# Performance work log

Hardware: AMD Instinct MI355X
Metric: run time of the kernel (lower is better)

## Reference

```python
import jax, jax.numpy as jnp
import numpy as np

H = 16
D_MODEL = 1024
D_K = D_MODEL // H


def setup_inputs() -> dict:
    key = jax.random.key(0)
    ks = jax.random.split(key, 11)
    B, S = 2, 2048
    scale = 1.0 / np.sqrt(D_MODEL)
    inp = {
        "query": jax.random.normal(ks[0], (B, S, D_MODEL), dtype=jnp.float32),
        "key": jax.random.normal(ks[1], (B, S, D_MODEL), dtype=jnp.float32),
        "value": jax.random.normal(ks[2], (B, S, D_MODEL), dtype=jnp.float32),
        "Wq": jax.random.normal(ks[3], (D_MODEL, D_MODEL), dtype=jnp.float32) * scale,
        "bq": jnp.zeros((D_MODEL,), dtype=jnp.float32),
        "Wk": jax.random.normal(ks[4], (D_MODEL, D_MODEL), dtype=jnp.float32) * scale,
        "bk": jnp.zeros((D_MODEL,), dtype=jnp.float32),
        "Wv": jax.random.normal(ks[5], (D_MODEL, D_MODEL), dtype=jnp.float32) * scale,
        "bv": jnp.zeros((D_MODEL,), dtype=jnp.float32),
        "Wo": jax.random.normal(ks[6], (D_MODEL, D_MODEL), dtype=jnp.float32) * scale,
        "bo": jnp.zeros((D_MODEL,), dtype=jnp.float32),
    }
    return inp


def _mha(query, key, value, Wq, bq, Wk, bk, Wv, bv, Wo, bo):
    B, S, _ = query.shape
    # linear projections (torch nn.Linear: x @ W.T + b)
    q = query @ Wq.T + bq
    k = key @ Wk.T + bk
    v = value @ Wv.T + bv
    # split heads: [B, S, D] -> [B, H, S, d_k]
    q = q.reshape(B, S, H, D_K).transpose(0, 2, 1, 3)
    k = k.reshape(B, S, H, D_K).transpose(0, 2, 1, 3)
    v = v.reshape(B, S, H, D_K).transpose(0, 2, 1, 3)
    # scaled dot-product attention with manual stable softmax
    scores = jnp.einsum("bhqd,bhkd->bhqk", q, k) / jnp.sqrt(jnp.float32(D_K))
    stable = scores - jnp.max(scores, axis=-1, keepdims=True)
    e = jnp.exp(stable)
    attn = e / jnp.sum(e, axis=-1, keepdims=True)
    ctx = jnp.einsum("bhqk,bhkd->bhqd", attn, v)
    # merge heads and final projection
    ctx = ctx.transpose(0, 2, 1, 3).reshape(B, S, H * D_K)
    return ctx @ Wo.T + bo


def reference(query, key, value, Wq, bq, Wk, bk, Wv, bv, Wo, bo):
    return _mha(query, key, value, Wq, bq, Wk, bk, Wv, bv, Wo, bo)
```

## Files before the change

### kernel.cpp

```cpp
#include <hip/hip_runtime.h>


#define S_LEN 2048
#define BATCH 2
#define DM    1024
#define NH    16
#define DKH   64
#define BS    (BATCH * S_LEN)

typedef _Float16 f16x8 __attribute__((ext_vector_type(8)));
typedef _Float16 f16x4 __attribute__((ext_vector_type(4)));
typedef _Float16 f16x2 __attribute__((ext_vector_type(2)));
typedef __fp16   h16x2 __attribute__((ext_vector_type(2)));
typedef float    f32x4 __attribute__((ext_vector_type(4)));

__device__ __forceinline__ f16x2 pk_f16(float a, float b) {
  h16x2 r = __builtin_amdgcn_cvt_pkrtz(a, b);
  return __builtin_bit_cast(f16x2, r);
}

__device__ __forceinline__ void gld16(const void* g, void* l) {
  __builtin_amdgcn_global_load_lds(
      (const __attribute__((address_space(1))) void*)g,
      (__attribute__((address_space(3))) void*)l, 16, 0, 0);
}

__device__ __forceinline__ float fast_exp2(float x) {
#if __has_builtin(__builtin_amdgcn_exp2f)
  return __builtin_amdgcn_exp2f(x);
#else
  return exp2f(x);
#endif
}

__global__ __launch_bounds__(256) void cvt_all(
    const float* __restrict__ q, const float* __restrict__ k, const float* __restrict__ v,
    const float* __restrict__ wq, const float* __restrict__ wk,
    const float* __restrict__ wv, const float* __restrict__ wo,
    _Float16* __restrict__ xq, _Float16* __restrict__ xk, _Float16* __restrict__ xv,
    _Float16* __restrict__ w16)
{
  const int y = blockIdx.y;
  const float* src; _Float16* dst; int n;
  if (y == 0)      { src = q;  dst = xq; n = BS * DM; }
  else if (y == 1) { src = k;  dst = xk; n = BS * DM; }
  else if (y == 2) { src = v;  dst = xv; n = BS * DM; }
  else {
    src = (y == 3) ? wq : ((y == 4) ? wk : ((y == 5) ? wv : wo));
    dst = w16 + (size_t)(y - 3) * (DM * DM);
    n = DM * DM;
  }
  int i0 = (blockIdx.x * 256 + threadIdx.x) * 4;
  if (i0 < n) {
    float4 f = *(const float4*)(src + i0);
    f16x2 lo = pk_f16(f.x, f.y);
    f16x2 hi = pk_f16(f.z, f.w);
    f16x4 h; h[0] = lo[0]; h[1] = lo[1]; h[2] = hi[0]; h[3] = hi[1];
    *(f16x4*)(dst + i0) = h;
  }
}

template <typename OUT_T, bool VT>
__device__ __forceinline__ void gemm_core(
    const _Float16* __restrict__ A, const _Float16* __restrict__ W,
    const float* __restrict__ bias, OUT_T* __restrict__ out, float oscale)
{
  const int tid  = threadIdx.x;
  const int l    = tid & 63;
  const int wv   = tid >> 6;
  const int c    = l & 15, quad = l >> 4;
  const int m0   = blockIdx.y * 128, n0 = blockIdx.x * 128;
  const int wm   = wv & 1, wn = wv >> 1;
  __shared__ _Float16 sA[128 * 64];
  __shared__ _Float16 sB[128 * 64];

  const _Float16* gA[4]; const _Float16* gB[4];
#pragma unroll
  for (int p = 0; p < 4; ++p) {
    int s = tid + p * 256, r = s >> 3, g = (s & 7) ^ (r & 7);
    gA[p] = A + (size_t)(m0 + r) * DM + g * 8;
    gB[p] = W + (size_t)(n0 + r) * DM + g * 8;
  }
  const int cx = c & 7;

  f32x4 acc[4][4] = {};
  for (int k0 = 0; k0 < DM; k0 += 64) {
    __syncthreads();
#pragma unroll
    for (int p = 0; p < 4; ++p) {
      gld16(gA[p] + k0, sA + (tid + p * 256) * 8);
      gld16(gB[p] + k0, sB + (tid + p * 256) * 8);
    }
    __syncthreads();
#pragma unroll
    for (int ks = 0; ks < 2; ++ks) {
      f16x8 af[4], bf[4];
#pragma unroll
      for (int i = 0; i < 4; ++i)
        af[i] = *(const f16x8*)&sA[(wm * 64 + i * 16 + c) * 64 + ((ks * 4 + quad) ^ cx) * 8];
#pragma unroll
      for (int j = 0; j < 4; ++j)
        bf[j] = *(const f16x8*)&sB[(wn * 64 + j * 16 + c) * 64 + ((ks * 4 + quad) ^ cx) * 8];
#pragma unroll
      for (int i = 0; i < 4; ++i)
#pragma unroll
        for (int j = 0; j < 4; ++j)
          acc[i][j] = __builtin_amdgcn_mfma_f32_16x16x32_f16(af[i], bf[j], acc[i][j], 0, 0, 0);
    }
  }
  if constexpr (VT) {
#pragma unroll
    for (int j = 0; j < 4; ++j) {
      int col = n0 + wn * 64 + j * 16 + c;
      float bb = bias[col];
      int hh = col >> 6, dd = col & 63;
#pragma unroll
      for (int i = 0; i < 4; ++i) {
        int row = m0 + wm * 64 + i * 16 + quad * 4;
        int bb2 = row >> 11, ss = row & (S_LEN - 1);
        _Float16* dst = (_Float16*)out + ((size_t)(bb2 * NH + hh) * DKH + dd) * S_LEN + ss;
        f16x4 v4;
#pragma unroll
        for (int r = 0; r < 4; ++r) v4[r] = (_Float16)((acc[i][j][r] + bb) * oscale);
        *(f16x4*)dst = v4;
      }
    }
  } else {
#pragma unroll
    for (int j = 0; j < 4; ++j) {
      int col = n0 + wn * 64 + j * 16 + c;
      float bb = bias[col];
#pragma unroll
      for (int i = 0; i < 4; ++i) {
        int row = m0 + wm * 64 + i * 16 + quad * 4;
#pragma unroll
        for (int r = 0; r < 4; ++r) {
          float vv = (acc[i][j][r] + bb) * oscale;
          out[(size_t)(row + r) * DM + col] = (OUT_T)vv;
        }
      }
    }
  }
}

#define SC_Q (0.125f * 1.44269504088896340736f)

__global__ __launch_bounds__(256) void proj3(
    const _Float16* __restrict__ xq, const _Float16* __restrict__ xk,
    const _Float16* __restrict__ xv, const _Float16* __restrict__ w16,
    const float* __restrict__ bq, const float* __restrict__ bk, const float* __restrict__ bv,
    _Float16* __restrict__ Q, _Float16* __restrict__ K, _Float16* __restrict__ Vt)
{
  const int z = blockIdx.z;
  if (z == 2) {
    gemm_core<_Float16, true>(xv, w16 + (size_t)2 * DM * DM, bv, Vt, 1.0f);
  } else if (z == 0) {
    gemm_core<_Float16, false>(xq, w16, bq, Q, SC_Q);
  } else {
    gemm_core<_Float16, false>(xk, w16 + (size_t)DM * DM, bk, K, 1.0f);
  }
}

__global__ __launch_bounds__(256) void out_gemm(
    const _Float16* __restrict__ ctx, const _Float16* __restrict__ wo,
    const float* __restrict__ bo, float* __restrict__ out)
{
  gemm_core<float, false>(ctx, wo, bo, out, 1.0f);
}

__global__ __launch_bounds__(256, 4) void attn(
    const _Float16* __restrict__ Q, const _Float16* __restrict__ K,
    const _Float16* __restrict__ Vt, _Float16* __restrict__ ctx)
{
  const int tid = threadIdx.x;
  const int l   = tid & 63, wv = tid >> 6;
  const int c   = l & 15, quad = l >> 4;
  const int q0  = blockIdx.x * 64;
  const int bh  = blockIdx.y;
  const int b   = bh >> 4, h = bh & 15;
  const int wq  = wv & 1, wd = wv >> 1;
  __shared__ _Float16 sK[2][64 * 64];
  __shared__ _Float16 sV[2][64 * 64];
  __shared__ _Float16 sP[64 * 64];

  f16x8 qf[4][2];
#pragma unroll
  for (int nt = 0; nt < 4; ++nt) {
    const _Float16* Qg = Q + ((size_t)(b * S_LEN + q0 + nt * 16 + c)) * DM + h * DKH;
    qf[nt][0] = *(const f16x8*)(Qg + quad * 8);
    qf[nt][1] = *(const f16x8*)(Qg + 32 + quad * 8);
  }

  f32x4 o[2][2] = {};
  float l_part[4] = {};
  const f16x2 ones = {(_Float16)1.0f, (_Float16)1.0f};

  const _Float16* Kg0 = K + ((size_t)b * S_LEN) * DM + h * DKH;
  const _Float16* Vg0 = Vt + ((size_t)bh * DKH) * S_LEN;

  const int sa = tid,       ra = sa >> 3, ba = (sa & 7) ^ (ra & 7);
  const int sb = tid + 256, rb = sb >> 3, bb = (sb & 7) ^ (rb & 7);
  const _Float16* gKa = Kg0 + (size_t)ra * DM + ba * 8;
  const _Float16* gKb = Kg0 + (size_t)rb * DM + bb * 8;
  const _Float16* gVa = Vg0 + (size_t)ra * S_LEN + ba * 8;
  const _Float16* gVb = Vg0 + (size_t)rb * S_LEN + bb * 8;
  const int cx = c & 7;

  gld16(gKa, sK[0] + sa * 8);
  gld16(gKb, sK[0] + sb * 8);
  gld16(gVa, sV[0] + sa * 8);
  gld16(gVb, sV[0] + sb * 8);
  __syncthreads();

  for (int kt = 0; kt < S_LEN / 64; ++kt) {
    const int cur = kt & 1;
    const int nk = (kt < S_LEN / 64 - 1) ? (kt + 1) : kt;
    const size_t k0n = (size_t)nk * 64;
    gld16(gKa + k0n * DM, sK[cur ^ 1] + sa * 8);
    gld16(gKb + k0n * DM, sK[cur ^ 1] + sb * 8);
    gld16(gVa + k0n,      sV[cur ^ 1] + sa * 8);
    gld16(gVb + k0n,      sV[cur ^ 1] + sb * 8);

    f32x4 sAcc[4] = {};
#pragma unroll
    for (int ks = 0; ks < 2; ++ks) {
      f16x8 kf = *(const f16x8*)&sK[cur][(wv * 16 + c) * 64 + ((ks * 4 + quad) ^ cx) * 8];
#pragma unroll
      for (int nt = 0; nt < 4; ++nt)
        sAcc[nt] = __builtin_amdgcn_mfma_f32_16x16x32_f16(kf, qf[nt][ks], sAcc[nt], 0, 0, 0);
    }

#pragma unroll
    for (int nt = 0; nt < 4; ++nt) {
      float p0 = fast_exp2(sAcc[nt][0]);
      float p1 = fast_exp2(sAcc[nt][1]);
      float p2 = fast_exp2(sAcc[nt][2]);
      float p3 = fast_exp2(sAcc[nt][3]);
      f16x2 lo = pk_f16(p0, p1);
      f16x2 hi = pk_f16(p2, p3);
      l_part[nt] = __builtin_amdgcn_fdot2(__builtin_bit_cast(h16x2, lo),
                                          __builtin_bit_cast(h16x2, ones), l_part[nt], false);
      l_part[nt] = __builtin_amdgcn_fdot2(__builtin_bit_cast(h16x2, hi),
                                          __builtin_bit_cast(h16x2, ones), l_part[nt], false);
      f16x4 pk; pk[0] = lo[0]; pk[1] = lo[1]; pk[2] = hi[0]; pk[3] = hi[1];
      int row = nt * 16 + c;
      int blk = (wv * 2 + (quad >> 1)) ^ (row & 7);
      *(f16x4*)&sP[row * 64 + blk * 8 + (quad & 1) * 4] = pk;
    }
    __syncthreads();

#pragma unroll
    for (int ks = 0; ks < 2; ++ks) {
      f16x8 af[2], bf[2];
#pragma unroll
      for (int qb = 0; qb < 2; ++qb) {
        int row = wq * 32 + qb * 16 + c;
        af[qb] = *(const f16x8*)&sP[row * 64 + ((ks * 4 + quad) ^ (row & 7)) * 8];
      }
#pragma unroll
      for (int db = 0; db < 2; ++db)
        bf[db] = *(const f16x8*)&sV[cur][(wd * 32 + db * 16 + c) * 64 + ((ks * 4 + quad) ^ cx) * 8];
#pragma unroll
      for (int qb = 0; qb < 2; ++qb)
#pragma unroll
        for (int db = 0; db < 2; ++db)
          o[qb][db] = __builtin_amdgcn_mfma_f32_16x16x32_f16(af[qb], bf[db], o[qb][db], 0, 0, 0);
    }
    __syncthreads();
  }

#pragma unroll
  for (int nt = 0; nt < 4; ++nt) {
    float s = l_part[nt];
    s += __shfl_xor(s, 16);
    s += __shfl_xor(s, 32);
    l_part[nt] = s;
  }
  float* lsum = (float*)&sK[0][0];
  if (quad == 0) {
#pragma unroll
    for (int nt = 0; nt < 4; ++nt) lsum[(nt * 16 + c) * 4 + wv] = l_part[nt];
  }
  __syncthreads();

#pragma unroll
  for (int qb = 0; qb < 2; ++qb) {
#pragma unroll
    for (int r = 0; r < 4; ++r) {
      int q = wq * 32 + qb * 16 + quad * 4 + r;
      f32x4 ls = *(const f32x4*)&lsum[q * 4];
      float inv = 1.0f / (ls[0] + ls[1] + ls[2] + ls[3]);
      _Float16* Og = ctx + ((size_t)(b * S_LEN + q0 + q)) * DM + h * DKH;
#pragma unroll
      for (int db = 0; db < 2; ++db)
        Og[wd * 32 + db * 16 + c] = (_Float16)(o[qb][db][r] * inv);
    }
  }
}

extern "C" void kernel_launch(void* const* d_in, const int* in_sizes, int n_in,
                              void* d_out, int out_size, void* d_ws, size_t ws_size,
                              hipStream_t stream)
{
  (void)in_sizes; (void)n_in; (void)out_size; (void)ws_size;
  const float* q  = (const float*)d_in[0];
  const float* k  = (const float*)d_in[1];
  const float* v  = (const float*)d_in[2];
  const float* wq = (const float*)d_in[3];
  const float* bq = (const float*)d_in[4];
  const float* wk = (const float*)d_in[5];
  const float* bk = (const float*)d_in[6];
  const float* wv = (const float*)d_in[7];
  const float* bv = (const float*)d_in[8];
  const float* wo = (const float*)d_in[9];
  const float* bo = (const float*)d_in[10];

  char* ws = (char*)d_ws;
  _Float16* XQ  = (_Float16*)(ws);
  _Float16* XK  = (_Float16*)(ws + (8u  << 20));
  _Float16* XV  = (_Float16*)(ws + (16u << 20));
  _Float16* W16 = (_Float16*)(ws + (24u << 20));
  _Float16* Qp  = (_Float16*)(ws + (32u << 20));
  _Float16* Kp  = (_Float16*)(ws + (40u << 20));
  _Float16* VT  = (_Float16*)(ws + (48u << 20));
  _Float16* CTX = XQ;
  float* out = (float*)d_out;

  cvt_all<<<dim3(4096, 7), 256, 0, stream>>>(q, k, v, wq, wk, wv, wo, XQ, XK, XV, W16);
  proj3<<<dim3(8, 32, 3), 256, 0, stream>>>(XQ, XK, XV, W16, bq, bk, bv, Qp, Kp, VT);
  attn<<<dim3(32, 32), 256, 0, stream>>>(Qp, Kp, VT, CTX);
  out_gemm<<<dim3(8, 32), 256, 0, stream>>>(CTX, W16 + (size_t)3 * DM * DM, bo, out);
}
```

Baseline: 234.3 us.

## Keep attention probabilities in registers using 32x32 MFMA with per-wave query rows

Rewrites the attention kernel so each wave owns 32 query rows (128 per block) and computes scores with 32x32x16 MFMA. The exp'd probabilities are then fed directly from registers into the PV MFMA, using a row permutation (swap23) on K loads so the accumulator layout matches the A-operand layout. This removes the shared-memory P buffer, one barrier per tile and the cross-wave row-sum reduction. In exchange it raises register pressure (occupancy hint lowered to 2) and halves the grid.

```diff
diff --git a/kernel.cpp b/kernel.cpp
--- a/kernel.cpp
+++ b/kernel.cpp
@@ -13,6 +13,7 @@
 typedef _Float16 f16x2 __attribute__((ext_vector_type(2)));
 typedef __fp16   h16x2 __attribute__((ext_vector_type(2)));
 typedef float    f32x4 __attribute__((ext_vector_type(4)));
+typedef float    f32x16 __attribute__((ext_vector_type(16)));
 
 __device__ __forceinline__ f16x2 pk_f16(float a, float b) {
   h16x2 r = __builtin_amdgcn_cvt_pkrtz(a, b);
@@ -31,6 +32,10 @@
 #else
   return exp2f(x);
 #endif
+}
+
+__device__ __forceinline__ int swap23(int x) {
+  return (x & ~12) | ((x & 4) << 1) | ((x & 8) >> 1);
 }
 
 __global__ __launch_bounds__(256) void cvt_all(
@@ -55,8 +60,8 @@
     float4 f = *(const float4*)(src + i0);
     f16x2 lo = pk_f16(f.x, f.y);
     f16x2 hi = pk_f16(f.z, f.w);
-    f16x4 h; h[0] = lo[0]; h[1] = lo[1]; h[2] = hi[0]; h[3] = hi[1];
-    *(f16x4*)(dst + i0) = h;
+    f16x4 hh; hh[0] = lo[0]; hh[1] = lo[1]; hh[2] = hi[0]; hh[3] = hi[1];
+    *(f16x4*)(dst + i0) = hh;
   }
 }
 
@@ -168,43 +173,40 @@
   gemm_core<float, false>(ctx, wo, bo, out, 1.0f);
 }
 
-__global__ __launch_bounds__(256, 4) void attn(
+__global__ __launch_bounds__(256, 2) void attn(
     const _Float16* __restrict__ Q, const _Float16* __restrict__ K,
     const _Float16* __restrict__ Vt, _Float16* __restrict__ ctx)
 {
   const int tid = threadIdx.x;
   const int l   = tid & 63, wv = tid >> 6;
-  const int c   = l & 15, quad = l >> 4;
-  const int q0  = blockIdx.x * 64;
+  const int lo5 = l & 31, hf = l >> 5;
+  const int q0  = blockIdx.x * 128;
   const int bh  = blockIdx.y;
-  const int b   = bh >> 4, h = bh & 15;
-  const int wq  = wv & 1, wd = wv >> 1;
+  const int b   = bh >> 4, hd = bh & 15;
   __shared__ _Float16 sK[2][64 * 64];
   __shared__ _Float16 sV[2][64 * 64];
-  __shared__ _Float16 sP[64 * 64];
-
-  f16x8 qf[4][2];
-#pragma unroll
-  for (int nt = 0; nt < 4; ++nt) {
-    const _Float16* Qg = Q + ((size_t)(b * S_LEN + q0 + nt * 16 + c)) * DM + h * DKH;
-    qf[nt][0] = *(const f16x8*)(Qg + quad * 8);
-    qf[nt][1] = *(const f16x8*)(Qg + 32 + quad * 8);
-  }
-
-  f32x4 o[2][2] = {};
-  float l_part[4] = {};
+
+  f16x8 qf[4];
+  {
+    const _Float16* Qg = Q + ((size_t)(b * S_LEN + q0 + wv * 32 + lo5)) * DM + hd * DKH + 8 * hf;
+#pragma unroll
+    for (int kc = 0; kc < 4; ++kc) qf[kc] = *(const f16x8*)(Qg + 16 * kc);
+  }
+
+  f32x16 o[2] = {};
+  float l_part = 0.f;
   const f16x2 ones = {(_Float16)1.0f, (_Float16)1.0f};
 
-  const _Float16* Kg0 = K + ((size_t)b * S_LEN) * DM + h * DKH;
+  const _Float16* Kg0 = K + ((size_t)b * S_LEN) * DM + hd * DKH;
   const _Float16* Vg0 = Vt + ((size_t)bh * DKH) * S_LEN;
 
   const int sa = tid,       ra = sa >> 3, ba = (sa & 7) ^ (ra & 7);
   const int sb = tid + 256, rb = sb >> 3, bb = (sb & 7) ^ (rb & 7);
-  const _Float16* gKa = Kg0 + (size_t)ra * DM + ba * 8;
-  const _Float16* gKb = Kg0 + (size_t)rb * DM + bb * 8;
+  const _Float16* gKa = Kg0 + (size_t)swap23(ra) * DM + ba * 8;
+  const _Float16* gKb = Kg0 + (size_t)swap23(rb) * DM + bb * 8;
   const _Float16* gVa = Vg0 + (size_t)ra * S_LEN + ba * 8;
   const _Float16* gVb = Vg0 + (size_t)rb * S_LEN + bb * 8;
-  const int cx = c & 7;
+  const int rx = lo5 & 7;
 
   gld16(gKa, sK[0] + sa * 8);
   gld16(gKb, sK[0] + sb * 8);
@@ -221,81 +223,60 @@
     gld16(gVa + k0n,      sV[cur ^ 1] + sa * 8);
     gld16(gVb + k0n,      sV[cur ^ 1] + sb * 8);
 
-    f32x4 sAcc[4] = {};
-#pragma unroll
-    for (int ks = 0; ks < 2; ++ks) {
-      f16x8 kf = *(const f16x8*)&sK[cur][(wv * 16 + c) * 64 + ((ks * 4 + quad) ^ cx) * 8];
-#pragma unroll
-      for (int nt = 0; nt < 4; ++nt)
-        sAcc[nt] = __builtin_amdgcn_mfma_f32_16x16x32_f16(kf, qf[nt][ks], sAcc[nt], 0, 0, 0);
-    }
-
-#pragma unroll
-    for (int nt = 0; nt < 4; ++nt) {
-      float p0 = fast_exp2(sAcc[nt][0]);
-      float p1 = fast_exp2(sAcc[nt][1]);
-      float p2 = fast_exp2(sAcc[nt][2]);
-      float p3 = fast_exp2(sAcc[nt][3]);
-      f16x2 lo = pk_f16(p0, p1);
-      f16x2 hi = pk_f16(p2, p3);
-      l_part[nt] = __builtin_amdgcn_fdot2(__builtin_bit_cast(h16x2, lo),
-                                          __builtin_bit_cast(h16x2, ones), l_part[nt], false);
-      l_part[nt] = __builtin_amdgcn_fdot2(__builtin_bit_cast(h16x2, hi),
-                                          __builtin_bit_cast(h16x2, ones), l_part[nt], false);
-      f16x4 pk; pk[0] = lo[0]; pk[1] = lo[1]; pk[2] = hi[0]; pk[3] = hi[1];
-      int row = nt * 16 + c;
-      int blk = (wv * 2 + (quad >> 1)) ^ (row & 7);
-      *(f16x4*)&sP[row * 64 + blk * 8 + (quad & 1) * 4] = pk;
-    }
+    f32x16 sAcc[2] = {};
+#pragma unroll
+    for (int kb = 0; kb < 2; ++kb)
+#pragma unroll
+      for (int kc = 0; kc < 4; ++kc) {
+        f16x8 kf = *(const f16x8*)&sK[cur][(32 * kb + lo5) * 64 + ((2 * kc + hf) ^ rx) * 8];
+        sAcc[kb] = __builtin_amdgcn_mfma_f32_32x32x16_f16(kf, qf[kc], sAcc[kb], 0, 0, 0);
+      }
+
+    f16x8 pPv[2][2];
+#pragma unroll
+    for (int kb = 0; kb < 2; ++kb)
+#pragma unroll
+      for (int half = 0; half < 2; ++half)
+#pragma unroll
+        for (int j2 = 0; j2 < 4; ++j2) {
+          float p0 = fast_exp2(sAcc[kb][8 * half + 2 * j2]);
+          float p1 = fast_exp2(sAcc[kb][8 * half + 2 * j2 + 1]);
+          f16x2 pk = pk_f16(p0, p1);
+          pPv[kb][half][2 * j2]     = pk[0];
+          pPv[kb][half][2 * j2 + 1] = pk[1];
+          l_part = __builtin_amdgcn_fdot2(__builtin_bit_cast(h16x2, pk),
+                                          __builtin_bit_cast(h16x2, ones), l_part, false);
+        }
+
+#pragma unroll
+    for (int db = 0; db < 2; ++db)
+#pragma unroll
+      for (int kc2 = 0; kc2 < 4; ++kc2) {
+        f16x8 vf = *(const f16x8*)&sV[cur][(32 * db + lo5) * 64 + ((2 * kc2 + hf) ^ rx) * 8];
+        o[db] = __builtin_amdgcn_mfma_f32_32x32x16_f16(pPv[kc2 >> 1][kc2 & 1], vf, o[db], 0, 0, 0);
+      }
+
     __syncthreads();
-
-#pragma unroll
-    for (int ks = 0; ks < 2; ++ks) {
-      f16x8 af[2], bf[2];
-#pragma unroll
-      for (int qb = 0; qb < 2; ++qb) {
-        int row = wq * 32 + qb * 16 + c;
-        af[qb] = *(const f16x8*)&sP[row * 64 + ((ks * 4 + quad) ^ (row & 7)) * 8];
-      }
-#pragma unroll
-      for (int db = 0; db < 2; ++db)
-        bf[db] = *(const f16x8*)&sV[cur][(wd * 32 + db * 16 + c) * 64 + ((ks * 4 + quad) ^ cx) * 8];
-#pragma unroll
-      for (int qb = 0; qb < 2; ++qb)
-#pragma unroll
-        for (int db = 0; db < 2; ++db)
-          o[qb][db] = __builtin_amdgcn_mfma_f32_16x16x32_f16(af[qb], bf[db], o[qb][db], 0, 0, 0);
-    }
-    __syncthreads();
-  }
-
-#pragma unroll
-  for (int nt = 0; nt < 4; ++nt) {
-    float s = l_part[nt];
-    s += __shfl_xor(s, 16);
-    s += __shfl_xor(s, 32);
-    l_part[nt] = s;
-  }
-  float* lsum = (float*)&sK[0][0];
-  if (quad == 0) {
-#pragma unroll
-    for (int nt = 0; nt < 4; ++nt) lsum[(nt * 16 + c) * 4 + wv] = l_part[nt];
-  }
-  __syncthreads();
-
-#pragma unroll
-  for (int qb = 0; qb < 2; ++qb) {
-#pragma unroll
-    for (int r = 0; r < 4; ++r) {
-      int q = wq * 32 + qb * 16 + quad * 4 + r;
-      f32x4 ls = *(const f32x4*)&lsum[q * 4];
-      float inv = 1.0f / (ls[0] + ls[1] + ls[2] + ls[3]);
-      _Float16* Og = ctx + ((size_t)(b * S_LEN + q0 + q)) * DM + h * DKH;
-#pragma unroll
-      for (int db = 0; db < 2; ++db)
-        Og[wd * 32 + db * 16 + c] = (_Float16)(o[qb][db][r] * inv);
-    }
-  }
+  }
+
+  l_part += __shfl_xor(l_part, 32);
+  float* lsum = (float*)&sK[0][0] + wv * 32;
+  if (hf == 0) lsum[lo5] = l_part;
+  float inv[16];
+#pragma unroll
+  for (int r = 0; r < 16; ++r) {
+    int qq = 8 * (r >> 2) + 4 * hf + (r & 3);
+    inv[r] = 1.0f / lsum[qq];
+  }
+
+  _Float16* Og = ctx + ((size_t)(b * S_LEN + q0 + wv * 32)) * DM + hd * DKH;
+#pragma unroll
+  for (int db = 0; db < 2; ++db)
+#pragma unroll
+    for (int r = 0; r < 16; ++r) {
+      int qq = 8 * (r >> 2) + 4 * hf + (r & 3);
+      Og[(size_t)qq * DM + 32 * db + lo5] = (_Float16)(o[db][r] * inv[r]);
+    }
 }
 
 extern "C" void kernel_launch(void* const* d_in, const int* in_sizes, int n_in,
@@ -328,6 +309,6 @@
 
   cvt_all<<<dim3(4096, 7), 256, 0, stream>>>(q, k, v, wq, wk, wv, wo, XQ, XK, XV, W16);
   proj3<<<dim3(8, 32, 3), 256, 0, stream>>>(XQ, XK, XV, W16, bq, bk, bv, Qp, Kp, VT);
-  attn<<<dim3(32, 32), 256, 0, stream>>>(Qp, Kp, VT, CTX);
+  attn<<<dim3(16, 32), 256, 0, stream>>>(Qp, Kp, VT, CTX);
   out_gemm<<<dim3(8, 32), 256, 0, stream>>>(CTX, W16 + (size_t)3 * DM * DM, bo, out);
 }
```

After: 226.5 us. 3.4% less time.
